# Performance work log

Hardware: AMD Instinct MI355X
Metric: run time of the kernel (lower is better)

The kernel has to match this reference:

```python
import jax, jax.numpy as jnp
import numpy as np

B, D, U = 8192, 1024, 1024

def setup_inputs() -> dict:
    key = jax.random.key(0)
    ks = jax.random.split(key, 20)
    s = 0.02
    inp = {
        'x': jax.random.normal(ks[0], (B, D), jnp.float32),
        'h': jax.random.normal(ks[1], (B, U), jnp.float32),
        'c': jax.random.normal(ks[2], (B, U), jnp.float32),
        'W_i': jax.random.normal(ks[3], (D, U), jnp.float32) * s,
        'W_f': jax.random.normal(ks[4], (D, U), jnp.float32) * s,
        'W_c': jax.random.normal(ks[5], (D, U), jnp.float32) * s,
        'W_o': jax.random.normal(ks[6], (D, U), jnp.float32) * s,
        'U_i': jax.random.normal(ks[7], (U, U), jnp.float32) * s,
        'U_f': jax.random.normal(ks[8], (U, U), jnp.float32) * s,
        'U_c': jax.random.normal(ks[9], (U, U), jnp.float32) * s,
        'U_o': jax.random.normal(ks[10], (U, U), jnp.float32) * s,
        'V_i': jnp.ones((U,), jnp.float32),
        'V_f': jnp.ones((U,), jnp.float32),
        'V_o': jnp.ones((U,), jnp.float32),
        'b_i': jnp.zeros((U,), jnp.float32),
        'b_f': jnp.ones((U,), jnp.float32),
        'b_c': jnp.zeros((U,), jnp.float32),
        'b_o': jnp.zeros((U,), jnp.float32),
    }
    return inp


def reference(x, h, c, W_i, W_f, W_c, W_o, U_i, U_f, U_c, U_o,
              V_i, V_f, V_o, b_i, b_f, b_c, b_o):
    # Fuse the 4 input and 4 recurrent projections into two GEMMs.
    W = jnp.concatenate([W_i, W_f, W_c, W_o], axis=1)   # [D, 4U]
    Uw = jnp.concatenate([U_i, U_f, U_c, U_o], axis=1)  # [U, 4U]
    b = jnp.concatenate([b_i, b_f, b_c, b_o])           # [4U]
    z = x @ W + h @ Uw + b                               # [B, 4U]
    zi, zf, zc, zo = jnp.split(z, 4, axis=1)
    i_t = jax.nn.sigmoid(zi + V_i * c)
    f_t = jax.nn.sigmoid(zf + V_f * c)
    c_tilde = jnp.tanh(zc)
    c_t = f_t * c + i_t * c_tilde
    o_t = jax.nn.sigmoid(zo + V_o * c_t)
    h_t = o_t * jnp.tanh(c_t)
    return (h_t, c_t)
```

## Files before the change

kernel.cpp:

```cpp
#include <hip/hip_runtime.h>
#include <hip/hip_bf16.h>
#include <stdint.h>


#define MM 8192
#define KK 2048
#define NN 4096
#define BM 128
#define BN 128
#define BK 64

typedef __attribute__((ext_vector_type(8))) __bf16 bf16x8;
typedef __attribute__((ext_vector_type(4))) float floatx4;
typedef __attribute__((ext_vector_type(8))) unsigned short ushort8_t;

__device__ __forceinline__ unsigned short f2bf(float f) {
    unsigned int u = __float_as_uint(f);
    u += 0x7FFF + ((u >> 16) & 1);
    return (unsigned short)(u >> 16);
}

__device__ __forceinline__ float fast_sigmoid(float x) {
    return 1.0f / (1.0f + __expf(-x));
}

__device__ __forceinline__ float fast_tanh(float x) {
    return 2.0f / (1.0f + __expf(-2.0f * x)) - 1.0f;
}

__device__ __forceinline__ void async_copy16(const void* g, void* l) {
    __builtin_amdgcn_global_load_lds(
        (const __attribute__((address_space(1))) void*)g,
        (__attribute__((address_space(3))) void*)l,
        16, 0, 0);
}

__global__ void pack_all(const float* __restrict__ x, const float* __restrict__ h,
                         const float* __restrict__ Wi, const float* __restrict__ Wf,
                         const float* __restrict__ Wc, const float* __restrict__ Wo,
                         const float* __restrict__ Ui, const float* __restrict__ Uf,
                         const float* __restrict__ Uc, const float* __restrict__ Uo,
                         unsigned short* __restrict__ A,
                         unsigned short* __restrict__ Wt) {
    __shared__ float tile[64][65];
    int blk = blockIdx.x;
    int tid = threadIdx.x;
    if (blk >= 2048) {
        int t = (blk - 2048) * 256 + tid;
        long base = (long)t * 8;
        int row = (int)(base >> 11);
        int col = (int)(base & 2047);
        const float* src = (col < 1024) ? (x + (long)row * 1024 + col)
                                        : (h + (long)row * 1024 + (col - 1024));
        float4 v0 = *(const float4*)src;
        float4 v1 = *(const float4*)(src + 4);
        ushort8_t o;
        o[0] = f2bf(v0.x); o[1] = f2bf(v0.y); o[2] = f2bf(v0.z); o[3] = f2bf(v0.w);
        o[4] = f2bf(v1.x); o[5] = f2bf(v1.y); o[6] = f2bf(v1.z); o[7] = f2bf(v1.w);
        *(ushort8_t*)(A + base) = o;
        return;
    }
    int z = blk >> 8;
    int rem = blk & 255;
    const float* src;
    switch (z) {
        case 0: src = Wi; break; case 1: src = Wf; break;
        case 2: src = Wc; break; case 3: src = Wo; break;
        case 4: src = Ui; break; case 5: src = Uf; break;
        case 6: src = Uc; break; default: src = Uo; break;
    }
    int g = z & 3;
    int koff = (z >= 4) ? 1024 : 0;
    int d0 = (rem >> 4) * 64;
    int u0 = (rem & 15) * 64;

    int j = tid & 63;
    int ib = tid >> 6;
#pragma unroll
    for (int p = 0; p < 16; ++p) {
        int i = p * 4 + ib;
        tile[i][j] = src[(long)(d0 + i) * 1024 + u0 + j];
    }
    __syncthreads();
    int i2 = (tid & 31) * 2;
    int jb = tid >> 5;
#pragma unroll
    for (int p = 0; p < 8; ++p) {
        int j2 = p * 8 + jb;
        unsigned short a = f2bf(tile[i2][j2]);
        unsigned short b = f2bf(tile[i2 + 1][j2]);
        long orow = (long)((u0 + j2) * 4 + g);
        *(ushort2*)(Wt + orow * 2048 + koff + d0 + i2) = make_ushort2(a, b);
    }
}

__global__ __launch_bounds__(256) void lstm_gemm(
    const unsigned short* __restrict__ A,
    const unsigned short* __restrict__ Wt,
    const float* __restrict__ c_in,
    const float* __restrict__ Vi, const float* __restrict__ Vf, const float* __restrict__ Vo,
    const float* __restrict__ bi_p, const float* __restrict__ bf_p,
    const float* __restrict__ bc_p, const float* __restrict__ bo_p,
    float* __restrict__ out) {
    __shared__ __align__(16) char smem[32768];
    unsigned short* As = (unsigned short*)smem;
    unsigned short* Bs = (unsigned short*)(smem + 16384);

    int tid = threadIdx.x;
    int wave = tid >> 6;
    int lane = tid & 63;
    int wm = wave >> 1, wn = wave & 1;

    int id = blockIdx.x;
    int bx = id & 63;
    int by = id >> 6;
    int rm0 = bx * BM;
    int cn0 = by * BN;

    int r_l = lane >> 3;
    int kc = ((lane & 7) ^ r_l) * 8;
    int voff = (wave * 32 + r_l) * 2048 + kc;
    const unsigned short* aP0 = A + (long)rm0 * 2048 + voff;
    const unsigned short* aP1 = aP0 + 8 * 2048;
    const unsigned short* aP2 = aP0 + 16 * 2048;
    const unsigned short* aP3 = aP0 + 24 * 2048;
    const unsigned short* bP0 = Wt + (long)cn0 * 2048 + voff;
    const unsigned short* bP1 = bP0 + 8 * 2048;
    const unsigned short* bP2 = bP0 + 16 * 2048;
    const unsigned short* bP3 = bP0 + 24 * 2048;
    char* ldsA = smem + wave * 4096;
    char* ldsB = smem + 16384 + wave * 4096;

    int fr = lane & 15;
    int fc = lane >> 4;
    int m7 = fr & 7;

    floatx4 acc[4][4];
#pragma unroll
    for (int i = 0; i < 4; ++i)
#pragma unroll
        for (int j = 0; j < 4; ++j) acc[i][j] = (floatx4)(0.0f);

#pragma unroll
    for (int kt = 0; kt < KK / BK; ++kt) {
        const int k0 = kt * BK;
        async_copy16(aP0 + k0, ldsA);
        async_copy16(aP1 + k0, ldsA + 1024);
        async_copy16(aP2 + k0, ldsA + 2048);
        async_copy16(aP3 + k0, ldsA + 3072);
        async_copy16(bP0 + k0, ldsB);
        async_copy16(bP1 + k0, ldsB + 1024);
        async_copy16(bP2 + k0, ldsB + 2048);
        async_copy16(bP3 + k0, ldsB + 3072);
        __syncthreads();

#pragma unroll
        for (int ks = 0; ks < 2; ++ks) {
            int sl = ((ks * 4 + fc) ^ m7) * 8;
            bf16x8 af[4], bfr[4];
#pragma unroll
            for (int mi = 0; mi < 4; ++mi)
                af[mi] = *(const bf16x8*)(As + (wm * 64 + mi * 16 + fr) * 64 + sl);
#pragma unroll
            for (int ni = 0; ni < 4; ++ni)
                bfr[ni] = *(const bf16x8*)(Bs + (wn * 64 + ni * 16 + fr) * 64 + sl);
#pragma unroll
            for (int mi = 0; mi < 4; ++mi)
#pragma unroll
                for (int ni = 0; ni < 4; ++ni)
                    acc[mi][ni] = __builtin_amdgcn_mfma_f32_16x16x32_bf16(
                        af[mi], bfr[ni], acc[mi][ni], 0, 0, 0);
        }
        __syncthreads();
    }

    float* zs = (float*)smem;
    int col = lane & 15;
    int q = lane >> 4;
    int u_b = tid & 31;
    int u_glob = by * 32 + u_b;
    float vVi = Vi[u_glob], vVf = Vf[u_glob], vVo = Vo[u_glob];
    float vbi = bi_p[u_glob], vbf = bf_p[u_glob], vbc = bc_p[u_glob], vbo = bo_p[u_glob];

#pragma unroll
    for (int mi = 0; mi < 4; ++mi) {
        if (mi) __syncthreads();
#pragma unroll
        for (int ni = 0; ni < 4; ++ni)
#pragma unroll
            for (int r = 0; r < 4; ++r)
                zs[(wm * 16 + q * 4 + r) * 132 + wn * 64 + ni * 16 + col] = acc[mi][ni][r];
        __syncthreads();
#pragma unroll
        for (int t = 0; t < 4; ++t) {
            int rowL = (tid >> 5) + t * 8;
            floatx4 z4 = *(const floatx4*)(zs + rowL * 132 + u_b * 4);
            long row_glob = rm0 + (rowL >> 4) * 64 + mi * 16 + (rowL & 15);
            float cv = c_in[row_glob * 1024 + u_glob];
            float i_t = fast_sigmoid(z4[0] + vbi + vVi * cv);
            float f_t = fast_sigmoid(z4[1] + vbf + vVf * cv);
            float ctl = fast_tanh(z4[2] + vbc);
            float c_t = f_t * cv + i_t * ctl;
            float o_t = fast_sigmoid(z4[3] + vbo + vVo * c_t);
            float h_t = o_t * fast_tanh(c_t);
            out[row_glob * 1024 + u_glob] = h_t;
            out[8388608 + row_glob * 1024 + u_glob] = c_t;
        }
    }
}

extern "C" void kernel_launch(void* const* d_in, const int* in_sizes, int n_in,
                              void* d_out, int out_size, void* d_ws, size_t ws_size,
                              hipStream_t stream) {
    const float* x  = (const float*)d_in[0];
    const float* h  = (const float*)d_in[1];
    const float* c  = (const float*)d_in[2];
    const float* Wi = (const float*)d_in[3];
    const float* Wf = (const float*)d_in[4];
    const float* Wc = (const float*)d_in[5];
    const float* Wo = (const float*)d_in[6];
    const float* Ui = (const float*)d_in[7];
    const float* Uf = (const float*)d_in[8];
    const float* Uc = (const float*)d_in[9];
    const float* Uo = (const float*)d_in[10];
    const float* Vi = (const float*)d_in[11];
    const float* Vf = (const float*)d_in[12];
    const float* Vo = (const float*)d_in[13];
    const float* bi = (const float*)d_in[14];
    const float* bf = (const float*)d_in[15];
    const float* bc = (const float*)d_in[16];
    const float* bo = (const float*)d_in[17];

    unsigned short* Abf = (unsigned short*)d_ws;
    unsigned short* Wt  = (unsigned short*)((char*)d_ws + 33554432);

    pack_all<<<dim3(10240), 256, 0, stream>>>(x, h, Wi, Wf, Wc, Wo,
                                              Ui, Uf, Uc, Uo, Abf, Wt);
    lstm_gemm<<<dim3(2048), 256, 0, stream>>>(Abf, Wt, c, Vi, Vf, Vo,
                                              bi, bf, bc, bo, (float*)d_out);
}
```

Baseline: 345.0 us.

## Rewrite LSTM GEMM as 256x256 tile with double-buffered async LDS pipeline

The fused GEMM moves from 128x128 tiles with 256 threads to 256x256 tiles with 512 threads. It uses a 128KB double-buffered LDS and an 8-phase schedule that interleaves async global-to-LDS loads with MFMA work, using explicit vmcnt waits and raw barriers. It also adds s_setprio around the MFMA bursts and an XCD-aware block swizzle. The goal is more data reuse per tile and hiding load latency behind compute, at the cost of heavy LDS use, high register pressure, and a complex barrier protocol that could limit occupancy.

```diff
diff --git a/kernel.cpp b/kernel.cpp
--- a/kernel.cpp
+++ b/kernel.cpp
@@ -6,8 +6,8 @@
 #define MM 8192
 #define KK 2048
 #define NN 4096
-#define BM 128
-#define BN 128
+#define BM 256
+#define BN 256
 #define BK 64
 
 typedef __attribute__((ext_vector_type(8))) __bf16 bf16x8;
@@ -94,7 +94,57 @@
     }
 }
 
-__global__ __launch_bounds__(256) void lstm_gemm(
+
+#define SBAR()  __builtin_amdgcn_s_barrier()
+#define WAITV4() asm volatile("s_waitcnt vmcnt(4)" ::: "memory")
+#define WAITV0() asm volatile("s_waitcnt vmcnt(0)" ::: "memory")
+#define WAITL0() asm volatile("s_waitcnt lgkmcnt(0)" ::: "memory")
+
+#define STAGE_A(BUF, HALF, KOFF) do { \
+    async_copy16(aG + (size_t)((HALF)*128) * 2048 + (KOFF), \
+                 smem + (BUF) + (HALF)*16384 + wave*1024); \
+    async_copy16(aG + (size_t)((HALF)*128 + 64) * 2048 + (KOFF), \
+                 smem + (BUF) + (HALF)*16384 + 8192 + wave*1024); \
+  } while (0)
+#define STAGE_B(BUF, HALF, KOFF) do { \
+    async_copy16(bG + (size_t)((HALF)*128) * 2048 + (KOFF), \
+                 smem + (BUF) + 32768 + (HALF)*16384 + wave*1024); \
+    async_copy16(bG + (size_t)((HALF)*128 + 64) * 2048 + (KOFF), \
+                 smem + (BUF) + 32768 + (HALF)*16384 + 8192 + wave*1024); \
+  } while (0)
+
+#define PHASE(BUF, MH, NH, STAGE_STMT, BND) do { \
+    bf16x8 af[4][2], bv[2][2]; \
+    _Pragma("unroll") \
+    for (int mi = 0; mi < 4; ++mi) { \
+      const char* ap = aR + (BUF) + ((MH)*128 + mi*16)*128; \
+      af[mi][0] = *(const bf16x8*)(ap + sl0); \
+      af[mi][1] = *(const bf16x8*)(ap + sl1); \
+    } \
+    _Pragma("unroll") \
+    for (int ni = 0; ni < 2; ++ni) { \
+      const char* bp = bR + (BUF) + ((NH)*128 + ni*16)*128; \
+      bv[ni][0] = *(const bf16x8*)(bp + sl0); \
+      bv[ni][1] = *(const bf16x8*)(bp + sl1); \
+    } \
+    STAGE_STMT; \
+    if (BND) { WAITV4(); } \
+    SBAR(); \
+    WAITL0(); \
+    __builtin_amdgcn_s_setprio(1); \
+    _Pragma("unroll") \
+    for (int ks = 0; ks < 2; ++ks) \
+      _Pragma("unroll") \
+      for (int mi = 0; mi < 4; ++mi) \
+        _Pragma("unroll") \
+        for (int ni = 0; ni < 2; ++ni) \
+          acc[MH][mi][NH][ni] = __builtin_amdgcn_mfma_f32_16x16x32_bf16( \
+              af[mi][ks], bv[ni][ks], acc[MH][mi][NH][ni], 0, 0, 0); \
+    __builtin_amdgcn_s_setprio(0); \
+    SBAR(); \
+  } while (0)
+
+__global__ __launch_bounds__(512, 2) void lstm_gemm(
     const unsigned short* __restrict__ A,
     const unsigned short* __restrict__ Wt,
     const float* __restrict__ c_in,
@@ -102,100 +152,92 @@
     const float* __restrict__ bi_p, const float* __restrict__ bf_p,
     const float* __restrict__ bc_p, const float* __restrict__ bo_p,
     float* __restrict__ out) {
-    __shared__ __align__(16) char smem[32768];
-    unsigned short* As = (unsigned short*)smem;
-    unsigned short* Bs = (unsigned short*)(smem + 16384);
+    __shared__ __align__(16) char smem[131072];
 
     int tid = threadIdx.x;
     int wave = tid >> 6;
     int lane = tid & 63;
-    int wm = wave >> 1, wn = wave & 1;
+    int wm = wave >> 2, wn = wave & 3;
+    int fr = lane & 15, fc = lane >> 4;
+    int m7 = fr & 7;
 
     int id = blockIdx.x;
-    int bx = id & 63;
-    int by = id >> 6;
+    int swz = (id & 7) * 64 + (id >> 3);
+    int bx = swz & 31;
+    int by = swz >> 5;
     int rm0 = bx * BM;
     int cn0 = by * BN;
 
     int r_l = lane >> 3;
-    int kc = ((lane & 7) ^ r_l) * 8;
-    int voff = (wave * 32 + r_l) * 2048 + kc;
-    const unsigned short* aP0 = A + (long)rm0 * 2048 + voff;
-    const unsigned short* aP1 = aP0 + 8 * 2048;
-    const unsigned short* aP2 = aP0 + 16 * 2048;
-    const unsigned short* aP3 = aP0 + 24 * 2048;
-    const unsigned short* bP0 = Wt + (long)cn0 * 2048 + voff;
-    const unsigned short* bP1 = bP0 + 8 * 2048;
-    const unsigned short* bP2 = bP0 + 16 * 2048;
-    const unsigned short* bP3 = bP0 + 24 * 2048;
-    char* ldsA = smem + wave * 4096;
-    char* ldsB = smem + 16384 + wave * 4096;
-
-    int fr = lane & 15;
-    int fc = lane >> 4;
-    int m7 = fr & 7;
-
-    floatx4 acc[4][4];
-#pragma unroll
-    for (int i = 0; i < 4; ++i)
-#pragma unroll
-        for (int j = 0; j < 4; ++j) acc[i][j] = (floatx4)(0.0f);
-
-#pragma unroll
-    for (int kt = 0; kt < KK / BK; ++kt) {
-        const int k0 = kt * BK;
-        async_copy16(aP0 + k0, ldsA);
-        async_copy16(aP1 + k0, ldsA + 1024);
-        async_copy16(aP2 + k0, ldsA + 2048);
-        async_copy16(aP3 + k0, ldsA + 3072);
-        async_copy16(bP0 + k0, ldsB);
-        async_copy16(bP1 + k0, ldsB + 1024);
-        async_copy16(bP2 + k0, ldsB + 2048);
-        async_copy16(bP3 + k0, ldsB + 3072);
-        __syncthreads();
-
-#pragma unroll
-        for (int ks = 0; ks < 2; ++ks) {
-            int sl = ((ks * 4 + fc) ^ m7) * 8;
-            bf16x8 af[4], bfr[4];
-#pragma unroll
-            for (int mi = 0; mi < 4; ++mi)
-                af[mi] = *(const bf16x8*)(As + (wm * 64 + mi * 16 + fr) * 64 + sl);
-#pragma unroll
-            for (int ni = 0; ni < 4; ++ni)
-                bfr[ni] = *(const bf16x8*)(Bs + (wn * 64 + ni * 16 + fr) * 64 + sl);
-#pragma unroll
-            for (int mi = 0; mi < 4; ++mi)
-#pragma unroll
-                for (int ni = 0; ni < 4; ++ni)
-                    acc[mi][ni] = __builtin_amdgcn_mfma_f32_16x16x32_bf16(
-                        af[mi], bfr[ni], acc[mi][ni], 0, 0, 0);
-        }
-        __syncthreads();
-    }
+    int csw = ((lane & 7) ^ r_l) * 8;
+    const unsigned short* aG = A  + (size_t)(rm0 + wave * 8 + r_l) * 2048 + csw;
+    const unsigned short* bG = Wt + (size_t)(cn0 + wave * 8 + r_l) * 2048 + csw;
+
+    int sl0 = (fc ^ m7) * 16;
+    int sl1 = ((4 + fc) ^ m7) * 16;
+    const char* aR = smem + (wm * 64 + fr) * 128;
+    const char* bR = smem + 32768 + (wn * 32 + fr) * 128;
+
+    floatx4 acc[2][4][2][2];
+#pragma unroll
+    for (int a0 = 0; a0 < 2; ++a0)
+#pragma unroll
+      for (int a1 = 0; a1 < 4; ++a1)
+#pragma unroll
+        for (int a2 = 0; a2 < 2; ++a2)
+#pragma unroll
+          for (int a3 = 0; a3 < 2; ++a3) acc[a0][a1][a2][a3] = (floatx4)(0.0f);
+
+    STAGE_B(0, 0, 0); STAGE_A(0, 0, 0); STAGE_B(0, 1, 0); STAGE_A(0, 1, 0);
+    STAGE_A(65536, 0, 64); STAGE_B(65536, 1, 64);
+    WAITV4();
+    SBAR();
+
+#pragma unroll 1
+    for (int it = 0; it < 16; ++it) {
+        int s0 = it * 2;
+        int kN1 = ((s0 + 1) & 31) * 64;
+        int kN2 = ((s0 + 2) & 31) * 64;
+        int kN3 = ((s0 + 3) & 31) * 64;
+        PHASE(0,     0, 0, STAGE_A(65536, 1, kN1), 0);
+        PHASE(0,     0, 1, STAGE_B(65536, 0, kN1), 0);
+        PHASE(0,     1, 1, STAGE_A(0,     0, kN2), 0);
+        PHASE(0,     1, 0, STAGE_B(0,     1, kN2), 1);
+        PHASE(65536, 0, 0, STAGE_A(0,     1, kN2), 0);
+        PHASE(65536, 0, 1, STAGE_B(0,     0, kN2), 0);
+        PHASE(65536, 1, 1, STAGE_A(65536, 0, kN3), 0);
+        PHASE(65536, 1, 0, STAGE_B(65536, 1, kN3), 1);
+    }
+
+    WAITV0();
+    SBAR();
 
     float* zs = (float*)smem;
-    int col = lane & 15;
-    int q = lane >> 4;
-    int u_b = tid & 31;
-    int u_glob = by * 32 + u_b;
+    int u_b = tid & 63;
+    int u_glob = (cn0 >> 2) + u_b;
     float vVi = Vi[u_glob], vVf = Vf[u_glob], vVo = Vo[u_glob];
     float vbi = bi_p[u_glob], vbf = bf_p[u_glob], vbc = bc_p[u_glob], vbo = bo_p[u_glob];
-
-#pragma unroll
-    for (int mi = 0; mi < 4; ++mi) {
-        if (mi) __syncthreads();
-#pragma unroll
-        for (int ni = 0; ni < 4; ++ni)
+    int zrb = tid >> 6;
+
+#pragma unroll
+    for (int mh = 0; mh < 2; ++mh)
+#pragma unroll
+      for (int mi = 0; mi < 4; ++mi) {
+        if (mh | mi) __syncthreads();
+#pragma unroll
+        for (int nh = 0; nh < 2; ++nh)
+#pragma unroll
+          for (int ni = 0; ni < 2; ++ni)
 #pragma unroll
             for (int r = 0; r < 4; ++r)
-                zs[(wm * 16 + q * 4 + r) * 132 + wn * 64 + ni * 16 + col] = acc[mi][ni][r];
+              zs[(wm * 16 + fc * 4 + r) * 260 + nh * 128 + wn * 32 + ni * 16 + fr] =
+                  acc[mh][mi][nh][ni][r];
         __syncthreads();
 #pragma unroll
         for (int t = 0; t < 4; ++t) {
-            int rowL = (tid >> 5) + t * 8;
-            floatx4 z4 = *(const floatx4*)(zs + rowL * 132 + u_b * 4);
-            long row_glob = rm0 + (rowL >> 4) * 64 + mi * 16 + (rowL & 15);
+            int zr = t * 8 + zrb;
+            floatx4 z4 = *(const floatx4*)(zs + zr * 260 + u_b * 4);
+            long row_glob = rm0 + mh * 128 + (zr >> 4) * 64 + mi * 16 + (zr & 15);
             float cv = c_in[row_glob * 1024 + u_glob];
             float i_t = fast_sigmoid(z4[0] + vbi + vVi * cv);
             float f_t = fast_sigmoid(z4[1] + vbf + vVf * cv);
@@ -206,7 +248,7 @@
             out[row_glob * 1024 + u_glob] = h_t;
             out[8388608 + row_glob * 1024 + u_glob] = c_t;
         }
-    }
+      }
 }
 
 extern "C" void kernel_launch(void* const* d_in, const int* in_sizes, int n_in,
@@ -236,6 +278,6 @@
 
     pack_all<<<dim3(10240), 256, 0, stream>>>(x, h, Wi, Wf, Wc, Wo,
                                               Ui, Uf, Uc, Uo, Abf, Wt);
-    lstm_gemm<<<dim3(2048), 256, 0, stream>>>(Abf, Wt, c, Vi, Vf, Vo,
-                                              bi, bf, bc, bo, (float*)d_out);
-}
+    lstm_gemm<<<dim3(512), 512, 0, stream>>>(Abf, Wt, c, Vi, Vf, Vo,
+                                             bi, bf, bc, bo, (float*)d_out);
+}
```

Measured after the change: 338.8 us. About the same (-1.8%).
